# Kernel tuning notes

Hardware: AMD Instinct MI355X
Metric: run time of the kernel (lower is better)

## Reference

```python
import jax, jax.numpy as jnp
import numpy as np

THRESHOLD = 0.99
B, M, H = 8, 2048, 1024


def setup_inputs():
    key = jax.random.key(0)
    ks = jax.random.split(key, 8)
    x = jax.random.normal(ks[0], (B, M, H), jnp.float32)
    run = jax.random.randint(ks[1], (B, M), 0, 2) > 0
    acc_p = jax.random.uniform(ks[2], (B, M, 1), jnp.float32) * 0.6
    weighted_h = jax.random.normal(ks[3], (B, M, H), jnp.float32)
    remainders = jnp.zeros((B, M, 1), jnp.float32)
    exit_ = jnp.zeros((B, M, 1), jnp.int32)
    pad_h = jax.random.normal(ks[4], (H,), jnp.float32)
    p_w = jax.random.normal(ks[5], (H, 1), jnp.float32) / np.sqrt(H)
    p_b = jnp.zeros((1,), jnp.float32)
    return {"x": x, "run": run, "acc_p": acc_p, "weighted_h": weighted_h,
            "remainders": remainders, "exit_": exit_, "updates": 3,
            "pad_h": pad_h, "p_w": p_w, "p_b": p_b}


def _unpack(x, run):
    # restore left-packed x to full [B, M, H] with zeros at non-run slots
    rank = jnp.cumsum(run, axis=1) - 1                      # [B, M] position in packed row
    g = jnp.take_along_axis(x, jnp.maximum(rank, 0)[..., None], axis=1)
    return jnp.where(run[..., None], g, jnp.zeros((), x.dtype))


def _pack(h, run, pad_h):
    # left-pack run tokens; tail slots get the pad vector (pad_ semantics).
    # Static-shape variant of torch pack: output is [B, M, H] (max_ <= M).
    order = jnp.argsort(~run, axis=1)                       # stable sort: run tokens first
    packed = jnp.take_along_axis(h, order[..., None], axis=1)
    counts = jnp.sum(run, axis=1, keepdims=True)            # [B, 1]
    valid = jnp.arange(run.shape[1])[None, :] < counts      # [B, M]
    return jnp.where(valid[..., None], packed, pad_h[None, None, :])


def reference(x, run, acc_p, weighted_h, remainders, exit_, updates, pad_h, p_w, p_b):
    runf = run[..., None].astype(x.dtype)                   # [B, M, 1]
    h = _unpack(x, run)                                     # [B, M, H]
    p = jax.nn.sigmoid(jnp.einsum('bmh,ho->bmo', h, p_w) + p_b) * runf
    mask_continue = ((acc_p + p) < THRESHOLD) & run[..., None]
    mask_exit = (~mask_continue) & run[..., None]
    mc = mask_continue.astype(x.dtype)
    me = mask_exit.astype(x.dtype)
    update = p * mc + (1.0 - acc_p) * me
    weighted_h_new = h * update + weighted_h
    run_new = run & mask_continue[..., 0]
    acc_p_new = acc_p + update * mc
    remainders_new = remainders + (1.0 - acc_p_new) * me
    updates_new = updates + 1
    exit_new = exit_ + updates_new * mask_exit.astype(exit_.dtype)
    h_packed = _pack(h, run_new, pad_h)
    return (h_packed, weighted_h_new, acc_p_new, remainders_new, run_new, exit_new)
```

## Files before the change

### kernel.cpp

```cpp
#include <hip/hip_runtime.h>

#define BB 8
#define MM 2048
#define HH 1024
#define THRESH 0.99f
#define BMH ((size_t)BB * MM * HH)
#define BM (BB * MM)
#define CHUNK 16
#define NBLK (BM / CHUNK)

typedef float f32x4 __attribute__((ext_vector_type(4)));

__device__ inline f32x4 ntload4(const float* p) {
    return __builtin_nontemporal_load((const f32x4*)p);
}
__device__ inline void ntstore4(float* p, f32x4 v) {
    __builtin_nontemporal_store(v, (f32x4*)p);
}
__device__ inline f32x4 ld4(const float* p) { return *(const f32x4*)p; }

__global__ __launch_bounds__(256) void phase1_kernel(
    const float* __restrict__ x, const int* __restrict__ run,
    const float* __restrict__ acc_p, const float* __restrict__ weighted_h,
    const float* __restrict__ remainders, const int* __restrict__ exit_,
    const int* __restrict__ updates, const float* __restrict__ p_w,
    const float* __restrict__ p_b,
    float* __restrict__ out_wh, float* __restrict__ out_accp,
    float* __restrict__ out_rem, float* __restrict__ out_run,
    float* __restrict__ out_exit, int* __restrict__ run_new_i,
    int* __restrict__ rank_ws) {
    __shared__ int wsum[4];
    __shared__ int cflag[CHUNK];
    __shared__ int crank[CHUNK];

    const int t0 = blockIdx.x * CHUNK;
    const int b  = t0 >> 11;
    const int m0 = t0 & (MM - 1);
    const int* rrow = run + b * MM;
    const int tid  = threadIdx.x;
    const int wave = tid >> 6;
    const int lane = tid & 63;

    f32x4 wv[4];
#pragma unroll
    for (int j = 0; j < 4; ++j) wv[j] = ld4(p_w + j * 256 + lane * 4);

    int s = 0;
    for (int i = tid; i < m0; i += 256) s += (rrow[i] != 0) ? 1 : 0;
#pragma unroll
    for (int off = 32; off > 0; off >>= 1) s += __shfl_xor(s, off, 64);
    if (lane == 0) wsum[wave] = s;
    if (tid < CHUNK) cflag[tid] = (rrow[m0 + tid] != 0) ? 1 : 0;
    __syncthreads();
    const int base0 = wsum[0] + wsum[1] + wsum[2] + wsum[3];
    if (tid < CHUNK) {
        int r = base0;
#pragma unroll
        for (int i = 0; i < CHUNK; ++i) r += (i <= tid) ? cflag[i] : 0;
        crank[tid] = r - 1;
        rank_ws[t0 + tid] = r - 1;
    }
    __syncthreads();

#pragma unroll
    for (int q = 0; q < 4; ++q) {
        const int ti = wave * 4 + q;
        const int t  = t0 + ti;
        const bool r = (cflag[ti] != 0);
        f32x4 hv[4];
        float dot = 0.f;
        if (r) {
            const float* xrow = x + ((size_t)(b * MM + crank[ti])) * HH;
#pragma unroll
            for (int j = 0; j < 4; ++j) {
                const int idx = j * 256 + lane * 4;
                hv[j] = ld4(xrow + idx);
                dot += hv[j].x * wv[j].x + hv[j].y * wv[j].y +
                       hv[j].z * wv[j].z + hv[j].w * wv[j].w;
            }
        } else {
#pragma unroll
            for (int j = 0; j < 4; ++j) hv[j] = (f32x4)(0.f);
        }
#pragma unroll
        for (int off = 32; off > 0; off >>= 1) dot += __shfl_xor(dot, off, 64);

        const float p = r ? (1.f / (1.f + expf(-(dot + p_b[0])))) : 0.f;
        const float ap = acc_p[t];
        const bool mc = r && ((ap + p) < THRESH);
        const bool me = r && !mc;
        const float upd = mc ? p : (me ? (1.f - ap) : 0.f);
        const float ap_new = mc ? (ap + p) : ap;

        const float* whrow = weighted_h + (size_t)t * HH;
        float* orow = out_wh + (size_t)t * HH;
#pragma unroll
        for (int j = 0; j < 4; ++j) {
            const int idx = j * 256 + lane * 4;
            const f32x4 w4 = ntload4(whrow + idx);
            f32x4 o = hv[j] * upd + w4;
            ntstore4(orow + idx, o);
        }
        if (lane == 0) {
            out_accp[t] = ap_new;
            out_rem[t]  = remainders[t] + (me ? (1.f - ap_new) : 0.f);
            out_run[t]  = mc ? 1.f : 0.f;
            out_exit[t] = (float)(exit_[t] + (me ? (updates[0] + 1) : 0));
            run_new_i[t] = mc ? 1 : 0;
        }
    }
}

__global__ __launch_bounds__(256) void phase2_kernel(
    const float* __restrict__ x, const float* __restrict__ pad_h,
    const int* __restrict__ run_new_i, const int* __restrict__ rank_ws,
    float* __restrict__ h_packed) {
    __shared__ int wsump[4];
    __shared__ int wsuma[4];
    __shared__ int cflag[CHUNK];
    __shared__ int crank2[CHUNK];

    const int t0 = blockIdx.x * CHUNK;
    const int b  = t0 >> 11;
    const int m0 = t0 & (MM - 1);
    const int* nrow = run_new_i + b * MM;
    const int tid  = threadIdx.x;
    const int wave = tid >> 6;
    const int lane = tid & 63;

    f32x4 pv[4];
#pragma unroll
    for (int j = 0; j < 4; ++j) pv[j] = ld4(pad_h + j * 256 + lane * 4);

    int sp = 0, sa = 0;
#pragma unroll
    for (int k = 0; k < MM / 256; ++k) {
        const int i = tid + k * 256;
        const int f = (nrow[i] != 0) ? 1 : 0;
        sa += f;
        if (i < m0) sp += f;
    }
#pragma unroll
    for (int off = 32; off > 0; off >>= 1) {
        sp += __shfl_xor(sp, off, 64);
        sa += __shfl_xor(sa, off, 64);
    }
    if (lane == 0) { wsump[wave] = sp; wsuma[wave] = sa; }
    if (tid < CHUNK) cflag[tid] = (nrow[m0 + tid] != 0) ? 1 : 0;
    __syncthreads();
    const int base0 = wsump[0] + wsump[1] + wsump[2] + wsump[3];
    const int cnt   = wsuma[0] + wsuma[1] + wsuma[2] + wsuma[3];
    if (tid < CHUNK) {
        int r = base0;
#pragma unroll
        for (int i = 0; i < CHUNK; ++i) r += (i <= tid) ? cflag[i] : 0;
        crank2[tid] = r - 1;
    }
    __syncthreads();

#pragma unroll
    for (int q = 0; q < 4; ++q) {
        const int ti = wave * 4 + q;
        const int t  = t0 + ti;
        const int m  = m0 + ti;
        if (cflag[ti] != 0) {
            const float* src = x + ((size_t)(b * MM + rank_ws[t])) * HH;
            float* dst = h_packed + ((size_t)(b * MM + crank2[ti])) * HH;
#pragma unroll
            for (int j = 0; j < 4; ++j) {
                const int idx = j * 256 + lane * 4;
                ntstore4(dst + idx, ld4(src + idx));
            }
        }
        if (m >= cnt) {
            float* prow = h_packed + (size_t)t * HH;
#pragma unroll
            for (int j = 0; j < 4; ++j) {
                const int idx = j * 256 + lane * 4;
                ntstore4(prow + idx, pv[j]);
            }
        }
    }
}

extern "C" void kernel_launch(void* const* d_in, const int* in_sizes, int n_in,
                              void* d_out, int out_size, void* d_ws, size_t ws_size,
                              hipStream_t stream) {
    const float* x          = (const float*)d_in[0];
    const int*   run        = (const int*)d_in[1];
    const float* acc_p      = (const float*)d_in[2];
    const float* weighted_h = (const float*)d_in[3];
    const float* remainders = (const float*)d_in[4];
    const int*   exit_      = (const int*)d_in[5];
    const int*   updates    = (const int*)d_in[6];
    const float* pad_h      = (const float*)d_in[7];
    const float* p_w        = (const float*)d_in[8];
    const float* p_b        = (const float*)d_in[9];

    float* out = (float*)d_out;
    float* out_hpacked = out;
    float* out_wh      = out + BMH;
    float* out_accp    = out + 2 * BMH;
    float* out_rem     = out_accp + BM;
    float* out_run     = out_rem + BM;
    float* out_exit    = out_run + BM;

    int* run_new_i = (int*)d_ws;
    int* rank_ws   = run_new_i + BM;

    phase1_kernel<<<NBLK, 256, 0, stream>>>(x, run, acc_p, weighted_h, remainders,
                                            exit_, updates, p_w, p_b,
                                            out_wh, out_accp, out_rem, out_run,
                                            out_exit, run_new_i, rank_ws);

    phase2_kernel<<<NBLK, 256, 0, stream>>>(x, pad_h, run_new_i, rank_ws,
                                            out_hpacked);
}
```

Before: 51.87 us.

## Split dot-product into prepass and fuse weighted update with packing

Computes the halting probabilities in a small first kernel that only reads x and writes p to workspace. A second kernel recomputes the continue mask and both ranks from run, acc_p and p, then does the weighted_h update and the packed-row scatter in one pass over x. This removes the separate packing kernel and its extra x row gather. In exchange, x rows are read in both kernels and each block redoes a full-row scan of three arrays.

```diff
diff --git a/kernel.cpp b/kernel.cpp
--- a/kernel.cpp
+++ b/kernel.cpp
@@ -19,16 +19,10 @@
 }
 __device__ inline f32x4 ld4(const float* p) { return *(const f32x4*)p; }
 
-__global__ __launch_bounds__(256) void phase1_kernel(
+__global__ __launch_bounds__(256) void dotp_kernel(
     const float* __restrict__ x, const int* __restrict__ run,
-    const float* __restrict__ acc_p, const float* __restrict__ weighted_h,
-    const float* __restrict__ remainders, const int* __restrict__ exit_,
-    const int* __restrict__ updates, const float* __restrict__ p_w,
-    const float* __restrict__ p_b,
-    float* __restrict__ out_wh, float* __restrict__ out_accp,
-    float* __restrict__ out_rem, float* __restrict__ out_run,
-    float* __restrict__ out_exit, int* __restrict__ run_new_i,
-    int* __restrict__ rank_ws) {
+    const float* __restrict__ p_w, const float* __restrict__ p_b,
+    float* __restrict__ p_ws) {
     __shared__ int wsum[4];
     __shared__ int cflag[CHUNK];
     __shared__ int crank[CHUNK];
@@ -58,7 +52,6 @@
 #pragma unroll
         for (int i = 0; i < CHUNK; ++i) r += (i <= tid) ? cflag[i] : 0;
         crank[tid] = r - 1;
-        rank_ws[t0 + tid] = r - 1;
     }
     __syncthreads();
 
@@ -67,117 +60,128 @@
         const int ti = wave * 4 + q;
         const int t  = t0 + ti;
         const bool r = (cflag[ti] != 0);
-        f32x4 hv[4];
         float dot = 0.f;
         if (r) {
             const float* xrow = x + ((size_t)(b * MM + crank[ti])) * HH;
 #pragma unroll
             for (int j = 0; j < 4; ++j) {
                 const int idx = j * 256 + lane * 4;
-                hv[j] = ld4(xrow + idx);
-                dot += hv[j].x * wv[j].x + hv[j].y * wv[j].y +
-                       hv[j].z * wv[j].z + hv[j].w * wv[j].w;
+                const f32x4 hv = ld4(xrow + idx);
+                dot += hv.x * wv[j].x + hv.y * wv[j].y +
+                       hv.z * wv[j].z + hv.w * wv[j].w;
             }
-        } else {
-#pragma unroll
-            for (int j = 0; j < 4; ++j) hv[j] = (f32x4)(0.f);
         }
 #pragma unroll
         for (int off = 32; off > 0; off >>= 1) dot += __shfl_xor(dot, off, 64);
-
-        const float p = r ? (1.f / (1.f + expf(-(dot + p_b[0])))) : 0.f;
-        const float ap = acc_p[t];
-        const bool mc = r && ((ap + p) < THRESH);
+        if (lane == 0)
+            p_ws[t] = r ? (1.f / (1.f + expf(-(dot + p_b[0])))) : 0.f;
+    }
+}
+
+__global__ __launch_bounds__(256) void main2_kernel(
+    const float* __restrict__ x, const int* __restrict__ run,
+    const float* __restrict__ acc_p, const float* __restrict__ weighted_h,
+    const float* __restrict__ remainders, const int* __restrict__ exit_,
+    const int* __restrict__ updates, const float* __restrict__ pad_h,
+    const float* __restrict__ p_ws,
+    float* __restrict__ out_hpacked, float* __restrict__ out_wh,
+    float* __restrict__ out_accp, float* __restrict__ out_rem,
+    float* __restrict__ out_run, float* __restrict__ out_exit) {
+    __shared__ int wsumR[4], wsumN[4], wsumA[4];
+    __shared__ int cflag[CHUNK], cnew[CHUNK];
+    __shared__ int crank[CHUNK], crank2[CHUNK];
+
+    const int t0 = blockIdx.x * CHUNK;
+    const int b  = t0 >> 11;
+    const int m0 = t0 & (MM - 1);
+    const int* rrow   = run   + b * MM;
+    const float* arow = acc_p + b * MM;
+    const float* prow = p_ws  + b * MM;
+    const int tid  = threadIdx.x;
+    const int wave = tid >> 6;
+    const int lane = tid & 63;
+
+    f32x4 pv[4];
+#pragma unroll
+    for (int j = 0; j < 4; ++j) pv[j] = ld4(pad_h + j * 256 + lane * 4);
+
+    int sR = 0, sN = 0, sA = 0;
+#pragma unroll
+    for (int k = 0; k < MM / 256; ++k) {
+        const int i = tid + k * 256;
+        const int f  = (rrow[i] != 0) ? 1 : 0;
+        const int mc = (f && (arow[i] + prow[i] < THRESH)) ? 1 : 0;
+        sA += mc;
+        if (i < m0) { sR += f; sN += mc; }
+    }
+#pragma unroll
+    for (int off = 32; off > 0; off >>= 1) {
+        sR += __shfl_xor(sR, off, 64);
+        sN += __shfl_xor(sN, off, 64);
+        sA += __shfl_xor(sA, off, 64);
+    }
+    if (lane == 0) { wsumR[wave] = sR; wsumN[wave] = sN; wsumA[wave] = sA; }
+    if (tid < CHUNK) {
+        const int f  = (rrow[m0 + tid] != 0) ? 1 : 0;
+        const int mc = (f && (arow[m0 + tid] + prow[m0 + tid] < THRESH)) ? 1 : 0;
+        cflag[tid] = f;
+        cnew[tid]  = mc;
+    }
+    __syncthreads();
+    const int baseR = wsumR[0] + wsumR[1] + wsumR[2] + wsumR[3];
+    const int baseN = wsumN[0] + wsumN[1] + wsumN[2] + wsumN[3];
+    const int cnt   = wsumA[0] + wsumA[1] + wsumA[2] + wsumA[3];
+    if (tid < CHUNK) {
+        int r = baseR, n = baseN;
+#pragma unroll
+        for (int i = 0; i < CHUNK; ++i) {
+            r += (i <= tid) ? cflag[i] : 0;
+            n += (i <= tid) ? cnew[i]  : 0;
+        }
+        crank[tid]  = r - 1;
+        crank2[tid] = n - 1;
+    }
+    __syncthreads();
+
+#pragma unroll
+    for (int q = 0; q < 4; ++q) {
+        const int ti = wave * 4 + q;
+        const int t  = t0 + ti;
+        const int m  = m0 + ti;
+        const bool r  = (cflag[ti] != 0);
+        const bool mc = (cnew[ti] != 0);
         const bool me = r && !mc;
+        const float p  = prow[m];
+        const float ap = arow[m];
         const float upd = mc ? p : (me ? (1.f - ap) : 0.f);
         const float ap_new = mc ? (ap + p) : ap;
 
+        const float* xrow  = x + ((size_t)(b * MM + crank[ti])) * HH;
+        float* dst = out_hpacked + ((size_t)(b * MM + crank2[ti])) * HH;
         const float* whrow = weighted_h + (size_t)t * HH;
         float* orow = out_wh + (size_t)t * HH;
+
 #pragma unroll
         for (int j = 0; j < 4; ++j) {
             const int idx = j * 256 + lane * 4;
             const f32x4 w4 = ntload4(whrow + idx);
-            f32x4 o = hv[j] * upd + w4;
-            ntstore4(orow + idx, o);
+            f32x4 hv = (f32x4)(0.f);
+            if (r) hv = ld4(xrow + idx);
+            ntstore4(orow + idx, hv * upd + w4);
+            if (mc) ntstore4(dst + idx, hv);
         }
         if (lane == 0) {
             out_accp[t] = ap_new;
             out_rem[t]  = remainders[t] + (me ? (1.f - ap_new) : 0.f);
             out_run[t]  = mc ? 1.f : 0.f;
             out_exit[t] = (float)(exit_[t] + (me ? (updates[0] + 1) : 0));
-            run_new_i[t] = mc ? 1 : 0;
-        }
-    }
-}
-
-__global__ __launch_bounds__(256) void phase2_kernel(
-    const float* __restrict__ x, const float* __restrict__ pad_h,
-    const int* __restrict__ run_new_i, const int* __restrict__ rank_ws,
-    float* __restrict__ h_packed) {
-    __shared__ int wsump[4];
-    __shared__ int wsuma[4];
-    __shared__ int cflag[CHUNK];
-    __shared__ int crank2[CHUNK];
-
-    const int t0 = blockIdx.x * CHUNK;
-    const int b  = t0 >> 11;
-    const int m0 = t0 & (MM - 1);
-    const int* nrow = run_new_i + b * MM;
-    const int tid  = threadIdx.x;
-    const int wave = tid >> 6;
-    const int lane = tid & 63;
-
-    f32x4 pv[4];
-#pragma unroll
-    for (int j = 0; j < 4; ++j) pv[j] = ld4(pad_h + j * 256 + lane * 4);
-
-    int sp = 0, sa = 0;
-#pragma unroll
-    for (int k = 0; k < MM / 256; ++k) {
-        const int i = tid + k * 256;
-        const int f = (nrow[i] != 0) ? 1 : 0;
-        sa += f;
-        if (i < m0) sp += f;
-    }
-#pragma unroll
-    for (int off = 32; off > 0; off >>= 1) {
-        sp += __shfl_xor(sp, off, 64);
-        sa += __shfl_xor(sa, off, 64);
-    }
-    if (lane == 0) { wsump[wave] = sp; wsuma[wave] = sa; }
-    if (tid < CHUNK) cflag[tid] = (nrow[m0 + tid] != 0) ? 1 : 0;
-    __syncthreads();
-    const int base0 = wsump[0] + wsump[1] + wsump[2] + wsump[3];
-    const int cnt   = wsuma[0] + wsuma[1] + wsuma[2] + wsuma[3];
-    if (tid < CHUNK) {
-        int r = base0;
-#pragma unroll
-        for (int i = 0; i < CHUNK; ++i) r += (i <= tid) ? cflag[i] : 0;
-        crank2[tid] = r - 1;
-    }
-    __syncthreads();
-
-#pragma unroll
-    for (int q = 0; q < 4; ++q) {
-        const int ti = wave * 4 + q;
-        const int t  = t0 + ti;
-        const int m  = m0 + ti;
-        if (cflag[ti] != 0) {
-            const float* src = x + ((size_t)(b * MM + rank_ws[t])) * HH;
-            float* dst = h_packed + ((size_t)(b * MM + crank2[ti])) * HH;
+        }
+        if (m >= cnt) {
+            float* padrow = out_hpacked + (size_t)t * HH;
 #pragma unroll
             for (int j = 0; j < 4; ++j) {
                 const int idx = j * 256 + lane * 4;
-                ntstore4(dst + idx, ld4(src + idx));
-            }
-        }
-        if (m >= cnt) {
-            float* prow = h_packed + (size_t)t * HH;
-#pragma unroll
-            for (int j = 0; j < 4; ++j) {
-                const int idx = j * 256 + lane * 4;
-                ntstore4(prow + idx, pv[j]);
+                ntstore4(padrow + idx, pv[j]);
             }
         }
     }
@@ -205,14 +209,12 @@
     float* out_run     = out_rem + BM;
     float* out_exit    = out_run + BM;
 
-    int* run_new_i = (int*)d_ws;
-    int* rank_ws   = run_new_i + BM;
-
-    phase1_kernel<<<NBLK, 256, 0, stream>>>(x, run, acc_p, weighted_h, remainders,
-                                            exit_, updates, p_w, p_b,
-                                            out_wh, out_accp, out_rem, out_run,
-                                            out_exit, run_new_i, rank_ws);
-
-    phase2_kernel<<<NBLK, 256, 0, stream>>>(x, pad_h, run_new_i, rank_ws,
-                                            out_hpacked);
-}
+    float* p_ws = (float*)d_ws;
+
+    dotp_kernel<<<NBLK, 256, 0, stream>>>(x, run, p_w, p_b, p_ws);
+
+    main2_kernel<<<NBLK, 256, 0, stream>>>(x, run, acc_p, weighted_h, remainders,
+                                           exit_, updates, pad_h, p_ws,
+                                           out_hpacked, out_wh, out_accp,
+                                           out_rem, out_run, out_exit);
+}
```

New measurement: 64.84 us. 25.0% more time.

## Fuse both phases into one kernel with cross-block mask flags

Applied to the files above, without the earlier changes.

Merges the compute kernel and the packing kernel into a single launch. Each block publishes a 16-bit continue-mask with a ready bit to workspace, then spins on the other blocks of its batch row to get the packed prefix count and total. The packing copy reuses x rows already hot in cache, and the run_new/rank workspace round trip and the second full-row scan disappear. It adds a memset launch and relies on every block of a row being co-resident for the spin-wait, so it risks deadlock or stalls if blocks are not all scheduled together.

```diff
diff --git a/kernel.cpp b/kernel.cpp
--- a/kernel.cpp
+++ b/kernel.cpp
@@ -7,7 +7,9 @@
 #define BMH ((size_t)BB * MM * HH)
 #define BM (BB * MM)
 #define CHUNK 16
+#define CPR (MM / CHUNK)
 #define NBLK (BM / CHUNK)
+#define RDY 0x40000000
 
 typedef float f32x4 __attribute__((ext_vector_type(4)));
 
@@ -19,23 +21,25 @@
 }
 __device__ inline f32x4 ld4(const float* p) { return *(const f32x4*)p; }
 
-__global__ __launch_bounds__(256) void phase1_kernel(
+__global__ __launch_bounds__(256, 4) void act_kernel(
     const float* __restrict__ x, const int* __restrict__ run,
     const float* __restrict__ acc_p, const float* __restrict__ weighted_h,
     const float* __restrict__ remainders, const int* __restrict__ exit_,
-    const int* __restrict__ updates, const float* __restrict__ p_w,
-    const float* __restrict__ p_b,
-    float* __restrict__ out_wh, float* __restrict__ out_accp,
-    float* __restrict__ out_rem, float* __restrict__ out_run,
-    float* __restrict__ out_exit, int* __restrict__ run_new_i,
-    int* __restrict__ rank_ws) {
+    const int* __restrict__ updates, const float* __restrict__ pad_h,
+    const float* __restrict__ p_w, const float* __restrict__ p_b,
+    float* __restrict__ out_hpacked, float* __restrict__ out_wh,
+    float* __restrict__ out_accp, float* __restrict__ out_rem,
+    float* __restrict__ out_run, float* __restrict__ out_exit,
+    int* __restrict__ mask_ws) {
     __shared__ int wsum[4];
-    __shared__ int cflag[CHUNK];
-    __shared__ int crank[CHUNK];
-
-    const int t0 = blockIdx.x * CHUNK;
-    const int b  = t0 >> 11;
-    const int m0 = t0 & (MM - 1);
+    __shared__ int cflag[CHUNK], cnew[CHUNK], crank[CHUNK], crank2[CHUNK];
+    __shared__ int rowmask[CPR];
+
+    const int chunk = blockIdx.x;
+    const int t0  = chunk * CHUNK;
+    const int b   = t0 >> 11;
+    const int m0  = t0 & (MM - 1);
+    const int myc = chunk & (CPR - 1);
     const int* rrow = run + b * MM;
     const int tid  = threadIdx.x;
     const int wave = tid >> 6;
@@ -58,10 +62,11 @@
 #pragma unroll
         for (int i = 0; i < CHUNK; ++i) r += (i <= tid) ? cflag[i] : 0;
         crank[tid] = r - 1;
-        rank_ws[t0 + tid] = r - 1;
-    }
-    __syncthreads();
-
+    }
+    __syncthreads();
+
+    const float pb = p_b[0];
+    const int upd1 = updates[0] + 1;
 #pragma unroll
     for (int q = 0; q < 4; ++q) {
         const int ti = wave * 4 + q;
@@ -85,7 +90,7 @@
 #pragma unroll
         for (int off = 32; off > 0; off >>= 1) dot += __shfl_xor(dot, off, 64);
 
-        const float p = r ? (1.f / (1.f + expf(-(dot + p_b[0])))) : 0.f;
+        const float p = r ? (1.f / (1.f + expf(-(dot + pb)))) : 0.f;
         const float ap = acc_p[t];
         const bool mc = r && ((ap + p) < THRESH);
         const bool me = r && !mc;
@@ -98,74 +103,63 @@
         for (int j = 0; j < 4; ++j) {
             const int idx = j * 256 + lane * 4;
             const f32x4 w4 = ntload4(whrow + idx);
-            f32x4 o = hv[j] * upd + w4;
-            ntstore4(orow + idx, o);
+            ntstore4(orow + idx, hv[j] * upd + w4);
         }
         if (lane == 0) {
             out_accp[t] = ap_new;
             out_rem[t]  = remainders[t] + (me ? (1.f - ap_new) : 0.f);
             out_run[t]  = mc ? 1.f : 0.f;
-            out_exit[t] = (float)(exit_[t] + (me ? (updates[0] + 1) : 0));
-            run_new_i[t] = mc ? 1 : 0;
-        }
-    }
-}
-
-__global__ __launch_bounds__(256) void phase2_kernel(
-    const float* __restrict__ x, const float* __restrict__ pad_h,
-    const int* __restrict__ run_new_i, const int* __restrict__ rank_ws,
-    float* __restrict__ h_packed) {
-    __shared__ int wsump[4];
-    __shared__ int wsuma[4];
-    __shared__ int cflag[CHUNK];
-    __shared__ int crank2[CHUNK];
-
-    const int t0 = blockIdx.x * CHUNK;
-    const int b  = t0 >> 11;
-    const int m0 = t0 & (MM - 1);
-    const int* nrow = run_new_i + b * MM;
-    const int tid  = threadIdx.x;
-    const int wave = tid >> 6;
-    const int lane = tid & 63;
+            out_exit[t] = (float)(exit_[t] + (me ? upd1 : 0));
+            cnew[ti] = mc ? 1 : 0;
+        }
+    }
+    __syncthreads();
+
+    if (tid == 0) {
+        int m16 = 0;
+#pragma unroll
+        for (int i = 0; i < CHUNK; ++i) m16 |= cnew[i] << i;
+        __hip_atomic_store(mask_ws + chunk, RDY | m16, __ATOMIC_RELAXED,
+                           __HIP_MEMORY_SCOPE_AGENT);
+    }
+
+    if (tid < CPR) {
+        const int* src = mask_ws + b * CPR + tid;
+        int v;
+        while (((v = __hip_atomic_load(src, __ATOMIC_RELAXED,
+                                       __HIP_MEMORY_SCOPE_AGENT)) & RDY) == 0) {
+            __builtin_amdgcn_s_sleep(4);
+        }
+        rowmask[tid] = v & 0xFFFF;
+    }
+    __syncthreads();
+
+    int baseN = 0, cnt = 0;
+    for (int c = 0; c < CPR; ++c) {
+        const int pc = __popc(rowmask[c]);
+        cnt += pc;
+        baseN += (c < myc) ? pc : 0;
+    }
+    if (tid < CHUNK) {
+        int n = baseN;
+#pragma unroll
+        for (int i = 0; i < CHUNK; ++i) n += (i <= tid) ? cnew[i] : 0;
+        crank2[tid] = n - 1;
+    }
+    __syncthreads();
 
     f32x4 pv[4];
 #pragma unroll
     for (int j = 0; j < 4; ++j) pv[j] = ld4(pad_h + j * 256 + lane * 4);
-
-    int sp = 0, sa = 0;
-#pragma unroll
-    for (int k = 0; k < MM / 256; ++k) {
-        const int i = tid + k * 256;
-        const int f = (nrow[i] != 0) ? 1 : 0;
-        sa += f;
-        if (i < m0) sp += f;
-    }
-#pragma unroll
-    for (int off = 32; off > 0; off >>= 1) {
-        sp += __shfl_xor(sp, off, 64);
-        sa += __shfl_xor(sa, off, 64);
-    }
-    if (lane == 0) { wsump[wave] = sp; wsuma[wave] = sa; }
-    if (tid < CHUNK) cflag[tid] = (nrow[m0 + tid] != 0) ? 1 : 0;
-    __syncthreads();
-    const int base0 = wsump[0] + wsump[1] + wsump[2] + wsump[3];
-    const int cnt   = wsuma[0] + wsuma[1] + wsuma[2] + wsuma[3];
-    if (tid < CHUNK) {
-        int r = base0;
-#pragma unroll
-        for (int i = 0; i < CHUNK; ++i) r += (i <= tid) ? cflag[i] : 0;
-        crank2[tid] = r - 1;
-    }
-    __syncthreads();
 
 #pragma unroll
     for (int q = 0; q < 4; ++q) {
         const int ti = wave * 4 + q;
         const int t  = t0 + ti;
         const int m  = m0 + ti;
-        if (cflag[ti] != 0) {
-            const float* src = x + ((size_t)(b * MM + rank_ws[t])) * HH;
-            float* dst = h_packed + ((size_t)(b * MM + crank2[ti])) * HH;
+        if (cnew[ti] != 0) {
+            const float* src = x + ((size_t)(b * MM + crank[ti])) * HH;
+            float* dst = out_hpacked + ((size_t)(b * MM + crank2[ti])) * HH;
 #pragma unroll
             for (int j = 0; j < 4; ++j) {
                 const int idx = j * 256 + lane * 4;
@@ -173,7 +167,7 @@
             }
         }
         if (m >= cnt) {
-            float* prow = h_packed + (size_t)t * HH;
+            float* prow = out_hpacked + (size_t)t * HH;
 #pragma unroll
             for (int j = 0; j < 4; ++j) {
                 const int idx = j * 256 + lane * 4;
@@ -205,14 +199,12 @@
     float* out_run     = out_rem + BM;
     float* out_exit    = out_run + BM;
 
-    int* run_new_i = (int*)d_ws;
-    int* rank_ws   = run_new_i + BM;
-
-    phase1_kernel<<<NBLK, 256, 0, stream>>>(x, run, acc_p, weighted_h, remainders,
-                                            exit_, updates, p_w, p_b,
-                                            out_wh, out_accp, out_rem, out_run,
-                                            out_exit, run_new_i, rank_ws);
-
-    phase2_kernel<<<NBLK, 256, 0, stream>>>(x, pad_h, run_new_i, rank_ws,
-                                            out_hpacked);
-}
+    int* mask_ws = (int*)d_ws;
+
+    hipMemsetAsync(mask_ws, 0, NBLK * sizeof(int), stream);
+
+    act_kernel<<<NBLK, 256, 0, stream>>>(x, run, acc_p, weighted_h, remainders,
+                                         exit_, updates, pad_h, p_w, p_b,
+                                         out_hpacked, out_wh, out_accp, out_rem,
+                                         out_run, out_exit, mask_ws);
+}
```

Result: slower. 57.31 us (+10.5%).
